# Optimization experiments

Measured on AMD Instinct MI355X. Metric: run time of the kernel, lower is better.

The kernel has to match this reference:

```python
import jax, jax.numpy as jnp
import numpy as np

B, S, D, H = 4, 1024, 1024, 16
HD = D // H  # 64
NEG = -10000000.0


def setup_inputs() -> dict:
    key = jax.random.key(0)
    ks = jax.random.split(key, 8)
    x = jax.random.normal(ks[0], (B, S, D), dtype=jnp.float32)
    adj = jax.random.randint(ks[1], (B, S, S), 0, 2).astype(jnp.float32)
    scale = 1.0 / np.sqrt(D)
    Wq = jax.random.normal(ks[2], (D, D), dtype=jnp.float32) * scale
    bq = jnp.zeros((D,), dtype=jnp.float32)
    Wk = jax.random.normal(ks[3], (D, D), dtype=jnp.float32) * scale
    bk = jnp.zeros((D,), dtype=jnp.float32)
    Wv = jax.random.normal(ks[4], (D, D), dtype=jnp.float32) * scale
    bv = jnp.zeros((D,), dtype=jnp.float32)
    return {"x": x, "adj": adj, "Wq": Wq, "bq": bq, "Wk": Wk, "bk": bk, "Wv": Wv, "bv": bv}


def reference(x, adj, Wq, bq, Wk, bk, Wv, bv):
    # QKV projections, split into heads: [B,S,D] -> [B,H,S,HD]
    def heads(t):
        return t.reshape(B, S, H, HD).transpose(0, 2, 1, 3)

    q = heads(x @ Wq + bq)
    k = heads(x @ Wk + bk)
    v = heads(x @ Wv + bv)

    # scaled scores [B,H,S,S]
    scores = jnp.einsum('bhqd,bhkd->bhqk', q, k) / jnp.sqrt(jnp.asarray(HD, x.dtype))
    # adjacency mask: 0 where adj>=0.5 else -1e7, broadcast over heads
    mask_add = jnp.where(adj < 0.5, jnp.asarray(NEG, x.dtype), jnp.asarray(0.0, x.dtype))
    scores = scores + mask_add[:, None, :, :]

    probs = jax.nn.softmax(scores, axis=-1)
    ctx = jnp.einsum('bhqk,bhkd->bhqd', probs, v)  # [B,H,S,HD]
    ctx = ctx.transpose(0, 2, 1, 3).reshape(B, S, D)
    h = jax.nn.relu(ctx)
    return (h, adj)
```

## Files before the change

### kernel.cpp

```cpp
#include <hip/hip_runtime.h>

constexpr int Bn  = 4;
constexpr int Sn  = 1024;
constexpr int Dn  = 1024;
constexpr int Hn  = 16;
constexpr int HDn = 64;

using short8   = __attribute__((ext_vector_type(8))) short;
using float4v  = __attribute__((ext_vector_type(4))) float;
using float16v = __attribute__((ext_vector_type(16))) float;

__device__ __forceinline__ ushort f2bf(float f) {
    union { float f; unsigned u; } v; v.f = f;
    unsigned r = v.u + 0x7fff + ((v.u >> 16) & 1);
    return (ushort)(r >> 16);
}

__device__ __forceinline__ void gload16(const void* g, void* l) {
    __builtin_amdgcn_global_load_lds(
        (const __attribute__((address_space(1))) void*)g,
        (__attribute__((address_space(3))) void*)l, 16, 0, 0);
}

__global__ __launch_bounds__(256) void convert_x(const float* __restrict__ x,
                                                 ushort* __restrict__ xb)
{
    const size_t i = ((size_t)blockIdx.x * 256 + threadIdx.x) * 8;
    float4 a = *(const float4*)&x[i];
    float4 b = *(const float4*)&x[i + 4];
    ushort o[8] = {f2bf(a.x), f2bf(a.y), f2bf(a.z), f2bf(a.w),
                   f2bf(b.x), f2bf(b.y), f2bf(b.z), f2bf(b.w)};
    *(uint4*)&xb[i] = *(const uint4*)o;
}

__global__ __launch_bounds__(256) void transpose_w(
    const float* __restrict__ Wq, const float* __restrict__ Wk,
    const float* __restrict__ Wv, ushort* __restrict__ Wt)
{
    const int which = blockIdx.z;
    const float* __restrict__ W = (which == 0) ? Wq : (which == 1) ? Wk : Wv;
    ushort* __restrict__ O = Wt + (size_t)which * Dn * Dn;

    const int k0 = blockIdx.x * 64;
    const int n0 = blockIdx.y * 64;
    const int t  = threadIdx.x;

    __shared__ __align__(16) ushort T[64][72];

    const int kl = t >> 4;
    const int nl = (t & 15) * 4;
#pragma unroll
    for (int p = 0; p < 4; ++p) {
        float4 w = *(const float4*)&W[(size_t)(k0 + p * 16 + kl) * Dn + n0 + nl];
        T[nl + 0][p * 16 + kl] = f2bf(w.x);
        T[nl + 1][p * 16 + kl] = f2bf(w.y);
        T[nl + 2][p * 16 + kl] = f2bf(w.z);
        T[nl + 3][p * 16 + kl] = f2bf(w.w);
    }
    __syncthreads();
    const int nr = t >> 2;
    const int kc = (t & 3) * 16;
    uint4 u0 = *(const uint4*)&T[nr][kc];
    uint4 u1 = *(const uint4*)&T[nr][kc + 8];
    *(uint4*)&O[(size_t)(n0 + nr) * Dn + k0 + kc]     = u0;
    *(uint4*)&O[(size_t)(n0 + nr) * Dn + k0 + kc + 8] = u1;
}

__global__ __launch_bounds__(256) void build_mask(const float* __restrict__ adj,
                                                  uint2* __restrict__ Mb)
{
    const int rid  = blockIdx.x * 256 + threadIdx.x;
    const int lane = rid & 63;
    const int w    = (rid >> 6) & 3;
    const int kt   = (rid >> 8) & 15;
    const int qt   = (rid >> 12) & 3;
    const int b    = rid >> 14;
    const int col  = lane & 31, hi = lane >> 5;

    unsigned bits[2] = {0u, 0u};
#pragma unroll
    for (int mt = 0; mt < 2; ++mt)
#pragma unroll
        for (int jt = 0; jt < 2; ++jt) {
            const int q = qt * 256 + w * 64 + jt * 32 + col;
            const float* row = adj + ((size_t)b * Sn + q) * Sn;
#pragma unroll
            for (int rg = 0; rg < 4; ++rg) {
                float4 a = *(const float4*)&row[kt * 64 + mt * 32 + rg * 8 + hi * 4];
                unsigned bb = (a.x >= 0.5f ? 1u : 0u) | (a.y >= 0.5f ? 2u : 0u) |
                              (a.z >= 0.5f ? 4u : 0u) | (a.w >= 0.5f ? 8u : 0u);
                bits[mt] |= bb << (jt * 16 + rg * 4);
            }
        }
    Mb[rid] = make_uint2(bits[0], bits[1]);
}

__global__ __launch_bounds__(256) void qkv_gemm(
    const ushort* __restrict__ xb, const ushort* __restrict__ Wt,
    const float* __restrict__ bq, const float* __restrict__ bk,
    const float* __restrict__ bv,
    ushort* __restrict__ Qb, ushort* __restrict__ Kb, ushort* __restrict__ Vb)
{
    const int which = blockIdx.z;
    const ushort* __restrict__ Bw   = Wt + (size_t)which * Dn * Dn;
    const float* __restrict__  bias = (which == 0) ? bq : (which == 1) ? bk : bv;
    ushort* __restrict__       Out  = (which == 0) ? Qb : (which == 1) ? Kb : Vb;
    const float scale = (which == 0) ? 0.125f : 1.0f;

    const int n0   = blockIdx.x * 128;
    const int m0   = blockIdx.y * 128;
    const int tid  = threadIdx.x;
    const int wave = tid >> 6;
    const int lane = tid & 63;
    const int wm   = wave >> 1;
    const int wn   = wave & 1;

    __shared__ __align__(16) ushort As[128 * 32];
    __shared__ __align__(16) ushort Bs[128 * 32];

    const int L0 = wave * 64 + lane;
    const int r0s = L0 >> 2, c0s = (L0 & 3) * 8;
    const int L1 = L0 + 256;
    const int r1s = L1 >> 2, c1s = (L1 & 3) * 8;

    const ushort* pA0 = &xb[(size_t)(m0 + r0s) * Dn + c0s];
    const ushort* pA1 = &xb[(size_t)(m0 + r1s) * Dn + c1s];
    const ushort* pB0 = &Bw[(size_t)(n0 + r0s) * Dn + c0s];
    const ushort* pB1 = &Bw[(size_t)(n0 + r1s) * Dn + c1s];

    char* ldsA0 = (char*)As + wave * 1024;
    char* ldsA1 = (char*)As + wave * 1024 + 4096;
    char* ldsB0 = (char*)Bs + wave * 1024;
    char* ldsB1 = (char*)Bs + wave * 1024 + 4096;

    const int mlane = lane & 15;
    const int kg    = (lane >> 4) * 8;

    float4v acc[4][4];
    const float4v z4 = {0.f, 0.f, 0.f, 0.f};
#pragma unroll
    for (int i = 0; i < 4; ++i)
#pragma unroll
        for (int j = 0; j < 4; ++j) acc[i][j] = z4;

    for (int k0 = 0; k0 < Dn; k0 += 32) {
        __syncthreads();
        gload16(pA0, ldsA0);
        gload16(pA1, ldsA1);
        gload16(pB0, ldsB0);
        gload16(pB1, ldsB1);
        pA0 += 32; pA1 += 32; pB0 += 32; pB1 += 32;
        __syncthreads();

        short8 af[4], bf[4];
#pragma unroll
        for (int i = 0; i < 4; ++i)
            af[i] = *(const short8*)&As[(wm * 64 + i * 16 + mlane) * 32 + kg];
#pragma unroll
        for (int j = 0; j < 4; ++j)
            bf[j] = *(const short8*)&Bs[(wn * 64 + j * 16 + mlane) * 32 + kg];
#pragma unroll
        for (int i = 0; i < 4; ++i)
#pragma unroll
            for (int j = 0; j < 4; ++j)
                acc[i][j] = __builtin_amdgcn_mfma_f32_16x16x32_bf16(af[i], bf[j], acc[i][j], 0, 0, 0);
    }

    const int rb  = (lane >> 4) * 4;
    const int col = lane & 15;
#pragma unroll
    for (int j = 0; j < 4; ++j) {
        const int n  = n0 + wn * 64 + j * 16 + col;
        const float bias_n = bias[n];
        const int h  = n >> 6;
        const int hd = n & 63;
#pragma unroll
        for (int i = 0; i < 4; ++i) {
#pragma unroll
            for (int r = 0; r < 4; ++r) {
                const int m = m0 + wm * 64 + i * 16 + rb + r;
                const int b = m >> 10;
                const int s = m & 1023;
                size_t addr;
                if (which == 2)
                    addr = (((size_t)(b * Hn + h)) * HDn + hd) * Sn + s;
                else
                    addr = (((size_t)(b * Hn + h)) * Sn + s) * HDn + hd;
                Out[addr] = f2bf((acc[i][j][r] + bias_n) * scale);
            }
        }
    }
}

__global__ __launch_bounds__(256, 1) void attn_mfma(
    const ushort* __restrict__ Q, const ushort* __restrict__ K,
    const ushort* __restrict__ Vt, const uint2* __restrict__ Mb,
    float* __restrict__ out)
{
    const int qt = blockIdx.x, h = blockIdx.y, b = blockIdx.z;
    const int tid  = threadIdx.x;
    const int w    = tid >> 6, lane = tid & 63;
    const int col  = lane & 31, hi = lane >> 5;

    const size_t hb = ((size_t)(b * Hn + h)) * Sn * HDn;
    const ushort* Kg = K + hb;
    const ushort* Vg = Vt + hb;

    __shared__ __align__(16) ushort Ks[2][64 * 72];
    __shared__ __align__(16) ushort Vs[2][64 * 72];

    short8 qf[2][4];
#pragma unroll
    for (int jt = 0; jt < 2; ++jt)
#pragma unroll
        for (int kp = 0; kp < 4; ++kp)
            qf[jt][kp] = *(const short8*)&Q[hb +
                (size_t)(qt * 256 + w * 64 + jt * 32 + col) * HDn + kp * 16 + hi * 8];

    float16v o_[2][2];
#pragma unroll
    for (int dt = 0; dt < 2; ++dt)
#pragma unroll
        for (int jt = 0; jt < 2; ++jt)
#pragma unroll
            for (int r = 0; r < 16; ++r) o_[dt][jt][r] = 0.f;
    float ls[2] = {0.f, 0.f};

    const int c0 = tid, c1 = tid + 256;
    const int la0 = (c0 >> 3) * 72 + (c0 & 7) * 8;
    const int la1 = (c1 >> 3) * 72 + (c1 & 7) * 8;

    uint4 k0 = *(const uint4*)&Kg[(size_t)(c0 >> 3) * HDn + (c0 & 7) * 8];
    uint4 k1 = *(const uint4*)&Kg[(size_t)(c1 >> 3) * HDn + (c1 & 7) * 8];
    uint4 v0 = *(const uint4*)&Vg[(size_t)(c0 >> 3) * Sn + (c0 & 7) * 8];
    uint4 v1 = *(const uint4*)&Vg[(size_t)(c1 >> 3) * Sn + (c1 & 7) * 8];
    *(uint4*)&Ks[0][la0] = k0;  *(uint4*)&Ks[0][la1] = k1;
    *(uint4*)&Vs[0][la0] = v0;  *(uint4*)&Vs[0][la1] = v1;
    __syncthreads();

    const uint2* mbase = Mb + ((size_t)(((b * 4 + qt) * 16) * 4 + w)) * 64 + lane;

    for (int kt = 0; kt < 16; ++kt) {
        const int cur = kt & 1;
        if (kt < 15) {
            k0 = *(const uint4*)&Kg[(size_t)((kt + 1) * 64 + (c0 >> 3)) * HDn + (c0 & 7) * 8];
            k1 = *(const uint4*)&Kg[(size_t)((kt + 1) * 64 + (c1 >> 3)) * HDn + (c1 & 7) * 8];
            v0 = *(const uint4*)&Vg[(size_t)(c0 >> 3) * Sn + (kt + 1) * 64 + (c0 & 7) * 8];
            v1 = *(const uint4*)&Vg[(size_t)(c1 >> 3) * Sn + (kt + 1) * 64 + (c1 & 7) * 8];
        }
        const uint2 m = mbase[(size_t)kt * 256];

#pragma unroll
        for (int mt = 0; mt < 2; ++mt) {
            float16v s_[2];
#pragma unroll
            for (int jt = 0; jt < 2; ++jt)
#pragma unroll
                for (int r = 0; r < 16; ++r) s_[jt][r] = 0.f;
#pragma unroll
            for (int kp = 0; kp < 4; ++kp) {
                short8 ak = *(const short8*)&Ks[cur][(mt * 32 + col) * 72 + kp * 16 + hi * 8];
                s_[0] = __builtin_amdgcn_mfma_f32_32x32x16_bf16(ak, qf[0][kp], s_[0], 0, 0, 0);
                s_[1] = __builtin_amdgcn_mfma_f32_32x32x16_bf16(ak, qf[1][kp], s_[1], 0, 0, 0);
            }

            const unsigned mw = (mt == 0) ? m.x : m.y;
            unsigned up[2][8];
#pragma unroll
            for (int jt = 0; jt < 2; ++jt) {
                float p[16];
#pragma unroll
                for (int r = 0; r < 16; ++r) {
                    const float e = __expf(s_[jt][r]);
                    p[r] = ((mw >> (jt * 16 + r)) & 1u) ? e : 0.0f;
                    ls[jt] += p[r];
                }
#pragma unroll
                for (int pr = 0; pr < 8; ++pr)
                    up[jt][pr] = (unsigned)f2bf(p[2 * pr]) | ((unsigned)f2bf(p[2 * pr + 1]) << 16);
            }

#pragma unroll
            for (int kh = 0; kh < 2; ++kh) {
                short8 pf[2];
#pragma unroll
                for (int jt = 0; jt < 2; ++jt) {
                    const unsigned a0 = up[jt][kh * 4 + 0], a1 = up[jt][kh * 4 + 1];
                    const unsigned a2 = up[jt][kh * 4 + 2], a3 = up[jt][kh * 4 + 3];
                    const unsigned t0 = (unsigned)__shfl_xor((int)(hi ? a0 : a2), 32, 64);
                    const unsigned t1 = (unsigned)__shfl_xor((int)(hi ? a1 : a3), 32, 64);
                    union { short8 s; unsigned u[4]; } f;
                    f.u[0] = hi ? t0 : a0;
                    f.u[1] = hi ? t1 : a1;
                    f.u[2] = hi ? a2 : t0;
                    f.u[3] = hi ? a3 : t1;
                    pf[jt] = f.s;
                }
                const int kp = mt * 2 + kh;
#pragma unroll
                for (int dt = 0; dt < 2; ++dt) {
                    short8 av = *(const short8*)&Vs[cur][(dt * 32 + col) * 72 + kp * 16 + hi * 8];
                    o_[dt][0] = __builtin_amdgcn_mfma_f32_32x32x16_bf16(av, pf[0], o_[dt][0], 0, 0, 0);
                    o_[dt][1] = __builtin_amdgcn_mfma_f32_32x32x16_bf16(av, pf[1], o_[dt][1], 0, 0, 0);
                }
            }
        }

        if (kt < 15) {
            const int nxt = cur ^ 1;
            *(uint4*)&Ks[nxt][la0] = k0;  *(uint4*)&Ks[nxt][la1] = k1;
            *(uint4*)&Vs[nxt][la0] = v0;  *(uint4*)&Vs[nxt][la1] = v1;
        }
        __syncthreads();
    }

#pragma unroll
    for (int jt = 0; jt < 2; ++jt) {
        float l = ls[jt] + (float)__shfl_xor((float)ls[jt], 32, 64);
        const float inv = 1.0f / l;
        const int q = qt * 256 + w * 64 + jt * 32 + col;
        float* op = &out[((size_t)b * Sn + q) * Dn + h * 64];
#pragma unroll
        for (int dt = 0; dt < 2; ++dt)
#pragma unroll
            for (int rg = 0; rg < 4; ++rg) {
                const int d = dt * 32 + rg * 8 + hi * 4;
                float4 o4;
                o4.x = fmaxf(o_[dt][jt][rg * 4 + 0] * inv, 0.0f);
                o4.y = fmaxf(o_[dt][jt][rg * 4 + 1] * inv, 0.0f);
                o4.z = fmaxf(o_[dt][jt][rg * 4 + 2] * inv, 0.0f);
                o4.w = fmaxf(o_[dt][jt][rg * 4 + 3] * inv, 0.0f);
                *(float4*)&op[d] = o4;
            }
    }
}

extern "C" void kernel_launch(void* const* d_in, const int* in_sizes, int n_in,
                              void* d_out, int out_size, void* d_ws, size_t ws_size,
                              hipStream_t stream)
{
    const float* x   = (const float*)d_in[0];
    const float* adj = (const float*)d_in[1];
    const float* Wq  = (const float*)d_in[2];
    const float* bq  = (const float*)d_in[3];
    const float* Wk  = (const float*)d_in[4];
    const float* bk  = (const float*)d_in[5];
    const float* Wv  = (const float*)d_in[6];
    const float* bv  = (const float*)d_in[7];
    float* out = (float*)d_out;

    ushort* xb = (ushort*)d_ws;
    ushort* Wt = xb + (size_t)Bn * Sn * Dn;
    ushort* Qb = Wt + (size_t)3 * Dn * Dn;
    ushort* Kb = Qb + (size_t)Bn * Hn * Sn * HDn;
    ushort* Vb = Kb + (size_t)Bn * Hn * Sn * HDn;
    uint2*  Mb = (uint2*)(Vb + (size_t)Bn * Hn * Sn * HDn);

    convert_x<<<dim3((Bn * Sn * Dn) / (256 * 8)), 256, 0, stream>>>(x, xb);
    transpose_w<<<dim3(16, 16, 3), 256, 0, stream>>>(Wq, Wk, Wv, Wt);
    build_mask<<<dim3((Bn * 4 * 16 * 4 * 64) / 256), 256, 0, stream>>>(adj, Mb);

    qkv_gemm<<<dim3(Dn / 128, (Bn * Sn) / 128, 3), 256, 0, stream>>>(
        xb, Wt, bq, bk, bv, Qb, Kb, Vb);

    attn_mfma<<<dim3(Sn / 256, Hn, Bn), 256, 0, stream>>>(Qb, Kb, Vb, Mb, out);

    hipMemcpyAsync(out + (size_t)Bn * Sn * Dn, adj,
                   (size_t)Bn * Sn * Sn * sizeof(float),
                   hipMemcpyDeviceToDevice, stream);
}
```

Before: 192.5 us.

## Merge prep kernels, halve attention query tile, use exp2 and precomputed word masks

```diff
diff --git a/kernel.cpp b/kernel.cpp
--- a/kernel.cpp
+++ b/kernel.cpp
@@ -22,77 +22,72 @@
         (__attribute__((address_space(3))) void*)l, 16, 0, 0);
 }
 
-__global__ __launch_bounds__(256) void convert_x(const float* __restrict__ x,
-                                                 ushort* __restrict__ xb)
+__global__ __launch_bounds__(256) void prep(
+    const float* __restrict__ x,
+    const float* __restrict__ Wq, const float* __restrict__ Wk,
+    const float* __restrict__ Wv, const float* __restrict__ adj,
+    ushort* __restrict__ xb, ushort* __restrict__ Wt, uint* __restrict__ Mb)
 {
-    const size_t i = ((size_t)blockIdx.x * 256 + threadIdx.x) * 8;
-    float4 a = *(const float4*)&x[i];
-    float4 b = *(const float4*)&x[i + 4];
-    ushort o[8] = {f2bf(a.x), f2bf(a.y), f2bf(a.z), f2bf(a.w),
-                   f2bf(b.x), f2bf(b.y), f2bf(b.z), f2bf(b.w)};
-    *(uint4*)&xb[i] = *(const uint4*)o;
-}
-
-__global__ __launch_bounds__(256) void transpose_w(
-    const float* __restrict__ Wq, const float* __restrict__ Wk,
-    const float* __restrict__ Wv, ushort* __restrict__ Wt)
-{
-    const int which = blockIdx.z;
-    const float* __restrict__ W = (which == 0) ? Wq : (which == 1) ? Wk : Wv;
-    ushort* __restrict__ O = Wt + (size_t)which * Dn * Dn;
-
-    const int k0 = blockIdx.x * 64;
-    const int n0 = blockIdx.y * 64;
-    const int t  = threadIdx.x;
-
-    __shared__ __align__(16) ushort T[64][72];
-
-    const int kl = t >> 4;
-    const int nl = (t & 15) * 4;
-#pragma unroll
-    for (int p = 0; p < 4; ++p) {
-        float4 w = *(const float4*)&W[(size_t)(k0 + p * 16 + kl) * Dn + n0 + nl];
-        T[nl + 0][p * 16 + kl] = f2bf(w.x);
-        T[nl + 1][p * 16 + kl] = f2bf(w.y);
-        T[nl + 2][p * 16 + kl] = f2bf(w.z);
-        T[nl + 3][p * 16 + kl] = f2bf(w.w);
+    const int bx  = blockIdx.x;
+    const int tid = threadIdx.x;
+    __shared__ __align__(16) ushort T[64 * 72];
+
+    if (bx < 2048) {
+        const size_t i = ((size_t)bx * 256 + tid) * 8;
+        float4 a = *(const float4*)&x[i];
+        float4 b = *(const float4*)&x[i + 4];
+        ushort o[8] = {f2bf(a.x), f2bf(a.y), f2bf(a.z), f2bf(a.w),
+                       f2bf(b.x), f2bf(b.y), f2bf(b.z), f2bf(b.w)};
+        *(uint4*)&xb[i] = *(const uint4*)o;
+    } else if (bx < 2816) {
+        const int idx = bx - 2048;
+        const int which = idx >> 8, rem = idx & 255;
+        const float* __restrict__ W = (which == 0) ? Wq : (which == 1) ? Wk : Wv;
+        ushort* __restrict__ O = Wt + (size_t)which * Dn * Dn;
+        const int k0 = (rem & 15) * 64, n0 = (rem >> 4) * 64;
+
+        const int kl = tid >> 4, nl = (tid & 15) * 4;
+#pragma unroll
+        for (int p = 0; p < 4; ++p) {
+            float4 w4 = *(const float4*)&W[(size_t)(k0 + p * 16 + kl) * Dn + n0 + nl];
+            T[(nl + 0) * 72 + p * 16 + kl] = f2bf(w4.x);
+            T[(nl + 1) * 72 + p * 16 + kl] = f2bf(w4.y);
+            T[(nl + 2) * 72 + p * 16 + kl] = f2bf(w4.z);
+            T[(nl + 3) * 72 + p * 16 + kl] = f2bf(w4.w);
+        }
+        __syncthreads();
+        const int nr = tid >> 2, kc = (tid & 3) * 16;
+        uint4 u0 = *(const uint4*)&T[nr * 72 + kc];
+        uint4 u1 = *(const uint4*)&T[nr * 72 + kc + 8];
+        *(uint4*)&O[(size_t)(n0 + nr) * Dn + k0 + kc]     = u0;
+        *(uint4*)&O[(size_t)(n0 + nr) * Dn + k0 + kc + 8] = u1;
+    } else {
+        const int rid  = (bx - 2816) * 256 + tid;
+        const int lane = rid & 63;
+        const int w    = (rid >> 6) & 3;
+        const int kt   = (rid >> 8) & 15;
+        const int qt   = (rid >> 12) & 7;
+        const int b    = rid >> 15;
+        const int col  = lane & 31, hi = lane >> 5;
+        const int q    = qt * 128 + w * 32 + col;
+        const float* arow = adj + ((size_t)b * Sn + q) * Sn + kt * 64;
+
+        uint words[16];
+#pragma unroll
+        for (int mt = 0; mt < 2; ++mt)
+#pragma unroll
+            for (int pr = 0; pr < 8; ++pr) {
+                const int r0 = 2 * pr;
+                const int k0l = mt * 32 + (r0 & 3) + 8 * (r0 >> 2) + 4 * hi;
+                float2 a = *(const float2*)&arow[k0l];
+                words[mt * 8 + pr] = (a.x >= 0.5f ? 0x0000FFFFu : 0u) |
+                                     (a.y >= 0.5f ? 0xFFFF0000u : 0u);
+            }
+        uint* dst = Mb + (size_t)rid * 16;
+#pragma unroll
+        for (int c = 0; c < 4; ++c)
+            *(uint4*)&dst[c * 4] = make_uint4(words[c*4], words[c*4+1], words[c*4+2], words[c*4+3]);
     }
-    __syncthreads();
-    const int nr = t >> 2;
-    const int kc = (t & 3) * 16;
-    uint4 u0 = *(const uint4*)&T[nr][kc];
-    uint4 u1 = *(const uint4*)&T[nr][kc + 8];
-    *(uint4*)&O[(size_t)(n0 + nr) * Dn + k0 + kc]     = u0;
-    *(uint4*)&O[(size_t)(n0 + nr) * Dn + k0 + kc + 8] = u1;
-}
-
-__global__ __launch_bounds__(256) void build_mask(const float* __restrict__ adj,
-                                                  uint2* __restrict__ Mb)
-{
-    const int rid  = blockIdx.x * 256 + threadIdx.x;
-    const int lane = rid & 63;
-    const int w    = (rid >> 6) & 3;
-    const int kt   = (rid >> 8) & 15;
-    const int qt   = (rid >> 12) & 3;
-    const int b    = rid >> 14;
-    const int col  = lane & 31, hi = lane >> 5;
-
-    unsigned bits[2] = {0u, 0u};
-#pragma unroll
-    for (int mt = 0; mt < 2; ++mt)
-#pragma unroll
-        for (int jt = 0; jt < 2; ++jt) {
-            const int q = qt * 256 + w * 64 + jt * 32 + col;
-            const float* row = adj + ((size_t)b * Sn + q) * Sn;
-#pragma unroll
-            for (int rg = 0; rg < 4; ++rg) {
-                float4 a = *(const float4*)&row[kt * 64 + mt * 32 + rg * 8 + hi * 4];
-                unsigned bb = (a.x >= 0.5f ? 1u : 0u) | (a.y >= 0.5f ? 2u : 0u) |
-                              (a.z >= 0.5f ? 4u : 0u) | (a.w >= 0.5f ? 8u : 0u);
-                bits[mt] |= bb << (jt * 16 + rg * 4);
-            }
-        }
-    Mb[rid] = make_uint2(bits[0], bits[1]);
 }
 
 __global__ __launch_bounds__(256) void qkv_gemm(
@@ -105,7 +100,7 @@
     const ushort* __restrict__ Bw   = Wt + (size_t)which * Dn * Dn;
     const float* __restrict__  bias = (which == 0) ? bq : (which == 1) ? bk : bv;
     ushort* __restrict__       Out  = (which == 0) ? Qb : (which == 1) ? Kb : Vb;
-    const float scale = (which == 0) ? 0.125f : 1.0f;
+    const float scale = (which == 0) ? 0.18033688011112042f : 1.0f;
 
     const int n0   = blockIdx.x * 128;
     const int m0   = blockIdx.y * 128;
@@ -192,9 +187,9 @@
     }
 }
 
-__global__ __launch_bounds__(256, 1) void attn_mfma(
+__global__ __launch_bounds__(256, 2) void attn_mfma(
     const ushort* __restrict__ Q, const ushort* __restrict__ K,
-    const ushort* __restrict__ Vt, const uint2* __restrict__ Mb,
+    const ushort* __restrict__ Vt, const uint* __restrict__ Mw,
     float* __restrict__ out)
 {
     const int qt = blockIdx.x, h = blockIdx.y, b = blockIdx.z;
@@ -209,22 +204,18 @@
     __shared__ __align__(16) ushort Ks[2][64 * 72];
     __shared__ __align__(16) ushort Vs[2][64 * 72];
 
-    short8 qf[2][4];
-#pragma unroll
-    for (int jt = 0; jt < 2; ++jt)
-#pragma unroll
-        for (int kp = 0; kp < 4; ++kp)
-            qf[jt][kp] = *(const short8*)&Q[hb +
-                (size_t)(qt * 256 + w * 64 + jt * 32 + col) * HDn + kp * 16 + hi * 8];
-
-    float16v o_[2][2];
+    short8 qf[4];
+#pragma unroll
+    for (int kp = 0; kp < 4; ++kp)
+        qf[kp] = *(const short8*)&Q[hb +
+            (size_t)(qt * 128 + w * 32 + col) * HDn + kp * 16 + hi * 8];
+
+    float16v o_[2];
 #pragma unroll
     for (int dt = 0; dt < 2; ++dt)
 #pragma unroll
-        for (int jt = 0; jt < 2; ++jt)
-#pragma unroll
-            for (int r = 0; r < 16; ++r) o_[dt][jt][r] = 0.f;
-    float ls[2] = {0.f, 0.f};
+        for (int r = 0; r < 16; ++r) o_[dt][r] = 0.f;
+    float ls = 0.f;
 
     const int c0 = tid, c1 = tid + 256;
     const int la0 = (c0 >> 3) * 72 + (c0 & 7) * 8;
@@ -238,7 +229,7 @@
     *(uint4*)&Vs[0][la0] = v0;  *(uint4*)&Vs[0][la1] = v1;
     __syncthreads();
 
-    const uint2* mbase = Mb + ((size_t)(((b * 4 + qt) * 16) * 4 + w)) * 64 + lane;
+    const uint* mbase = Mw + ((size_t)((b * 8 + qt) * 16) * 4 + w) * 1024 + lane * 16;
 
     for (int kt = 0; kt < 16; ++kt) {
         const int cur = kt & 1;
@@ -248,60 +239,51 @@
             v0 = *(const uint4*)&Vg[(size_t)(c0 >> 3) * Sn + (kt + 1) * 64 + (c0 & 7) * 8];
             v1 = *(const uint4*)&Vg[(size_t)(c1 >> 3) * Sn + (kt + 1) * 64 + (c1 & 7) * 8];
         }
-        const uint2 m = mbase[(size_t)kt * 256];
+        const uint* mp = mbase + (size_t)kt * 4096;
+        uint4 mk4[4];
+        mk4[0] = *(const uint4*)(mp);
+        mk4[1] = *(const uint4*)(mp + 4);
+        mk4[2] = *(const uint4*)(mp + 8);
+        mk4[3] = *(const uint4*)(mp + 12);
+        const uint* mka = (const uint*)mk4;
 
 #pragma unroll
         for (int mt = 0; mt < 2; ++mt) {
-            float16v s_[2];
-#pragma unroll
-            for (int jt = 0; jt < 2; ++jt)
-#pragma unroll
-                for (int r = 0; r < 16; ++r) s_[jt][r] = 0.f;
+            float16v s_;
+#pragma unroll
+            for (int r = 0; r < 16; ++r) s_[r] = 0.f;
 #pragma unroll
             for (int kp = 0; kp < 4; ++kp) {
                 short8 ak = *(const short8*)&Ks[cur][(mt * 32 + col) * 72 + kp * 16 + hi * 8];
-                s_[0] = __builtin_amdgcn_mfma_f32_32x32x16_bf16(ak, qf[0][kp], s_[0], 0, 0, 0);
-                s_[1] = __builtin_amdgcn_mfma_f32_32x32x16_bf16(ak, qf[1][kp], s_[1], 0, 0, 0);
-            }
-
-            const unsigned mw = (mt == 0) ? m.x : m.y;
-            unsigned up[2][8];
-#pragma unroll
-            for (int jt = 0; jt < 2; ++jt) {
-                float p[16];
-#pragma unroll
-                for (int r = 0; r < 16; ++r) {
-                    const float e = __expf(s_[jt][r]);
-                    p[r] = ((mw >> (jt * 16 + r)) & 1u) ? e : 0.0f;
-                    ls[jt] += p[r];
-                }
-#pragma unroll
-                for (int pr = 0; pr < 8; ++pr)
-                    up[jt][pr] = (unsigned)f2bf(p[2 * pr]) | ((unsigned)f2bf(p[2 * pr + 1]) << 16);
+                s_ = __builtin_amdgcn_mfma_f32_32x32x16_bf16(ak, qf[kp], s_, 0, 0, 0);
+            }
+
+            unsigned up[8];
+#pragma unroll
+            for (int pr = 0; pr < 8; ++pr) {
+                const unsigned e0 = __float_as_uint(exp2f(s_[2 * pr]))     + 0x8000u;
+                const unsigned e1 = __float_as_uint(exp2f(s_[2 * pr + 1])) + 0x8000u;
+                const unsigned u  = __builtin_amdgcn_perm(e1, e0, 0x07060302u) & mka[mt * 8 + pr];
+                up[pr] = u;
+                ls += __uint_as_float(u << 16) + __uint_as_float(u & 0xffff0000u);
             }
 
 #pragma unroll
             for (int kh = 0; kh < 2; ++kh) {
-                short8 pf[2];
-#pragma unroll
-                for (int jt = 0; jt < 2; ++jt) {
-                    const unsigned a0 = up[jt][kh * 4 + 0], a1 = up[jt][kh * 4 + 1];
-                    const unsigned a2 = up[jt][kh * 4 + 2], a3 = up[jt][kh * 4 + 3];
-                    const unsigned t0 = (unsigned)__shfl_xor((int)(hi ? a0 : a2), 32, 64);
-                    const unsigned t1 = (unsigned)__shfl_xor((int)(hi ? a1 : a3), 32, 64);
-                    union { short8 s; unsigned u[4]; } f;
-                    f.u[0] = hi ? t0 : a0;
-                    f.u[1] = hi ? t1 : a1;
-                    f.u[2] = hi ? a2 : t0;
-                    f.u[3] = hi ? a3 : t1;
-                    pf[jt] = f.s;
-                }
+                const unsigned a0 = up[kh * 4 + 0], a1 = up[kh * 4 + 1];
+                const unsigned a2 = up[kh * 4 + 2], a3 = up[kh * 4 + 3];
+                const unsigned t0 = (unsigned)__shfl_xor((int)(hi ? a0 : a2), 32, 64);
+                const unsigned t1 = (unsigned)__shfl_xor((int)(hi ? a1 : a3), 32, 64);
+                union { short8 s; unsigned u[4]; } f;
+                f.u[0] = hi ? t0 : a0;
+                f.u[1] = hi ? t1 : a1;
+                f.u[2] = hi ? a2 : t0;
+                f.u[3] = hi ? a3 : t1;
                 const int kp = mt * 2 + kh;
 #pragma unroll
                 for (int dt = 0; dt < 2; ++dt) {
                     short8 av = *(const short8*)&Vs[cur][(dt * 32 + col) * 72 + kp * 16 + hi * 8];
-                    o_[dt][0] = __builtin_amdgcn_mfma_f32_32x32x16_bf16(av, pf[0], o_[dt][0], 0, 0, 0);
-                    o_[dt][1] = __builtin_amdgcn_mfma_f32_32x32x16_bf16(av, pf[1], o_[dt][1], 0, 0, 0);
+                    o_[dt] = __builtin_amdgcn_mfma_f32_32x32x16_bf16(av, f.s, o_[dt], 0, 0, 0);
                 }
             }
         }
@@ -314,25 +296,22 @@
         __syncthreads();
     }
 
-#pragma unroll
-    for (int jt = 0; jt < 2; ++jt) {
-        float l = ls[jt] + (float)__shfl_xor((float)ls[jt], 32, 64);
-        const float inv = 1.0f / l;
-        const int q = qt * 256 + w * 64 + jt * 32 + col;
-        float* op = &out[((size_t)b * Sn + q) * Dn + h * 64];
-#pragma unroll
-        for (int dt = 0; dt < 2; ++dt)
-#pragma unroll
-            for (int rg = 0; rg < 4; ++rg) {
-                const int d = dt * 32 + rg * 8 + hi * 4;
-                float4 o4;
-                o4.x = fmaxf(o_[dt][jt][rg * 4 + 0] * inv, 0.0f);
-                o4.y = fmaxf(o_[dt][jt][rg * 4 + 1] * inv, 0.0f);
-                o4.z = fmaxf(o_[dt][jt][rg * 4 + 2] * inv, 0.0f);
-                o4.w = fmaxf(o_[dt][jt][rg * 4 + 3] * inv, 0.0f);
-                *(float4*)&op[d] = o4;
-            }
-    }
+    float l = ls + (float)__shfl_xor((float)ls, 32, 64);
+    const float inv = 1.0f / l;
+    const int q = qt * 128 + w * 32 + col;
+    float* op = &out[((size_t)b * Sn + q) * Dn + h * 64];
+#pragma unroll
+    for (int dt = 0; dt < 2; ++dt)
+#pragma unroll
+        for (int rg = 0; rg < 4; ++rg) {
+            const int d = dt * 32 + rg * 8 + hi * 4;
+            float4 o4;
+            o4.x = fmaxf(o_[dt][rg * 4 + 0] * inv, 0.0f);
+            o4.y = fmaxf(o_[dt][rg * 4 + 1] * inv, 0.0f);
+            o4.z = fmaxf(o_[dt][rg * 4 + 2] * inv, 0.0f);
+            o4.w = fmaxf(o_[dt][rg * 4 + 3] * inv, 0.0f);
+            *(float4*)&op[d] = o4;
+        }
 }
 
 extern "C" void kernel_launch(void* const* d_in, const int* in_sizes, int n_in,
@@ -354,16 +333,14 @@
     ushort* Qb = Wt + (size_t)3 * Dn * Dn;
     ushort* Kb = Qb + (size_t)Bn * Hn * Sn * HDn;
     ushort* Vb = Kb + (size_t)Bn * Hn * Sn * HDn;
-    uint2*  Mb = (uint2*)(Vb + (size_t)Bn * Hn * Sn * HDn);
-
-    convert_x<<<dim3((Bn * Sn * Dn) / (256 * 8)), 256, 0, stream>>>(x, xb);
-    transpose_w<<<dim3(16, 16, 3), 256, 0, stream>>>(Wq, Wk, Wv, Wt);
-    build_mask<<<dim3((Bn * 4 * 16 * 4 * 64) / 256), 256, 0, stream>>>(adj, Mb);
+    uint*   Mb = (uint*)(Vb + (size_t)Bn * Hn * Sn * HDn);
+
+    prep<<<dim3(3328), 256, 0, stream>>>(x, Wq, Wk, Wv, adj, xb, Wt, Mb);
 
     qkv_gemm<<<dim3(Dn / 128, (Bn * Sn) / 128, 3), 256, 0, stream>>>(
         xb, Wt, bq, bk, bv, Qb, Kb, Vb);
 
-    attn_mfma<<<dim3(Sn / 256, Hn, Bn), 256, 0, stream>>>(Qb, Kb, Vb, Mb, out);
+    attn_mfma<<<dim3(8, Hn, Bn), 256, 0, stream>>>(Qb, Kb, Vb, Mb, out);
 
     hipMemcpyAsync(out + (size_t)Bn * Sn * Dn, adj,
                    (size_t)Bn * Sn * Sn * sizeof(float),
```

New measurement: 191.0 us. No clear change (-0.8%).
